# Optimization experiments

Hardware: AMD Instinct MI355X
Metric: run time of the kernel (lower is better)

## Reference

```python
import jax, jax.numpy as jnp
import numpy as np

T, B, D_IN, H = 512, 256, 64, 128


def _normc(key, shape):
    w = jax.random.normal(key, shape, dtype=jnp.float32)
    return w / jnp.sqrt(jnp.sum(w * w, axis=1, keepdims=True))


def setup_inputs() -> dict:
    key = jax.random.key(0)
    ks = jax.random.split(key, 8)
    state = jax.random.normal(ks[0], (T, B, D_IN), dtype=jnp.float32)
    # PyTorch LSTMCell params: weight_ih [4H, in], weight_hh [4H, H], biases [4H]
    s = 1.0 / np.sqrt(H)
    W_ih0 = jax.random.uniform(ks[1], (4 * H, D_IN), minval=-s, maxval=s, dtype=jnp.float32)
    W_hh0 = jax.random.uniform(ks[2], (4 * H, H), minval=-s, maxval=s, dtype=jnp.float32)
    b_ih0 = jnp.zeros((4 * H,), jnp.float32)
    b_hh0 = jnp.zeros((4 * H,), jnp.float32)
    W_ih1 = jax.random.uniform(ks[3], (4 * H, H), minval=-s, maxval=s, dtype=jnp.float32)
    W_hh1 = jax.random.uniform(ks[4], (4 * H, H), minval=-s, maxval=s, dtype=jnp.float32)
    b_ih1 = jnp.zeros((4 * H,), jnp.float32)
    b_hh1 = jnp.zeros((4 * H,), jnp.float32)
    # normc-initialized output head (rows normalized to unit norm, zero bias)
    W_out = _normc(ks[5], (1, H))
    b_out = jnp.zeros((1,), jnp.float32)
    return dict(state=state, W_ih0=W_ih0, W_hh0=W_hh0, b_ih0=b_ih0, b_hh0=b_hh0,
                W_ih1=W_ih1, W_hh1=W_hh1, b_ih1=b_ih1, b_hh1=b_hh1,
                W_out=W_out, b_out=b_out)


def _lstm_cell(x, h, c, W_ih, W_hh, b_ih, b_hh):
    # gates: [B, 4H], chunk order i, f, g, o (PyTorch convention)
    g = x @ W_ih.T + b_ih + h @ W_hh.T + b_hh
    i, f, gg, o = jnp.split(g, 4, axis=-1)
    i = jax.nn.sigmoid(i)
    f = jax.nn.sigmoid(f)
    gg = jnp.tanh(gg)
    o = jax.nn.sigmoid(o)
    c2 = f * c + i * gg
    h2 = o * jnp.tanh(c2)
    return h2, c2


def reference(state, W_ih0, W_hh0, b_ih0, b_hh0, W_ih1, W_hh1, b_ih1, b_hh1, W_out, b_out):
    Bsz = state.shape[1]
    Hd = W_hh0.shape[1]
    z = jnp.zeros((Bsz, Hd), state.dtype)

    def step(carry, x_t):
        h0, c0, h1, c1 = carry
        h0, c0 = _lstm_cell(x_t, h0, c0, W_ih0, W_hh0, b_ih0, b_hh0)
        h1, c1 = _lstm_cell(h0, h1, c1, W_ih1, W_hh1, b_ih1, b_hh1)
        v_t = h1 @ W_out.T + b_out  # [B, 1]
        return (h0, c0, h1, c1), v_t

    _, values = jax.lax.scan(step, (z, z, z, z), state)
    return values  # [T, B, 1]
```

## Files before the change

kernel.cpp:

```cpp
#include <hip/hip_runtime.h>


#define T_STEPS 512
#define BATCH   256
#define DIN     64
#define GROUP   16
#define NGRP    (T_STEPS / GROUP)

typedef _Float16 half8 __attribute__((ext_vector_type(8)));
typedef float    f32x4 __attribute__((ext_vector_type(4)));

#define LOG2E  1.44269504088896f
#define LOG2E2 2.88539008177793f

#define WH_IH0 0
#define WH_HH0 32768
#define WH_IH1 98304
#define WH_HH1 163840
#define WH_X2     229376
#define WH_SLAB2  8617984
#define WB_FLAG2  50790400
#define WS2_TOTAL 50823168
#define WH_SLAB1  229376
#define WB_FLAG1  34013184
#define WS1_TOTAL 34045952
#define WS0XH_TOTAL ((size_t)(WH_X2 + 8388608) * 2)

__global__ void prep_weights(const float* __restrict__ wih0,
                             const float* __restrict__ whh0,
                             const float* __restrict__ wih1,
                             const float* __restrict__ whh1,
                             _Float16* __restrict__ ws) {
    int idx = blockIdx.x * 256 + threadIdx.x;
    float v; int row;
    if (idx < 32768)       { row = idx >> 6;             v = wih0[idx]; }
    else if (idx < 98304)  { row = (idx - 32768) >> 7;   v = whh0[idx - 32768]; }
    else if (idx < 163840) { row = (idx - 98304) >> 7;   v = wih1[idx - 98304]; }
    else                   { row = (idx - 163840) >> 7;  v = whh1[idx - 163840]; }
    float sc = ((row >> 7) == 2) ? LOG2E2 : LOG2E;
    ws[idx] = (_Float16)(v * sc);
}

__global__ void prep_state(const float* __restrict__ s, _Float16* __restrict__ d) {
    int i = (blockIdx.x * 256 + threadIdx.x) * 8;
    f32x4 a = *(const f32x4*)(s + i);
    f32x4 b = *(const f32x4*)(s + i + 4);
    half8 h;
    h[0]=(_Float16)a[0]; h[1]=(_Float16)a[1]; h[2]=(_Float16)a[2]; h[3]=(_Float16)a[3];
    h[4]=(_Float16)b[0]; h[5]=(_Float16)b[1]; h[6]=(_Float16)b[2]; h[7]=(_Float16)b[3];
    *(half8*)(d + i) = h;
}

__device__ __forceinline__ float sig2(float y) {
    return __builtin_amdgcn_rcpf(1.0f + __builtin_amdgcn_exp2f(-y));
}
__device__ __forceinline__ float tanh2(float y2) {
    return 1.0f - 2.0f * __builtin_amdgcn_rcpf(1.0f + __builtin_amdgcn_exp2f(y2));
}
__device__ __forceinline__ float tanh_c(float c) {
    return 1.0f - 2.0f * __builtin_amdgcn_rcpf(1.0f + __builtin_amdgcn_exp2f(c * LOG2E2));
}

#define PIPE_LDS_BYTES ((65536 + 4096 + 128) * 2)

template<bool XH>
__global__ __launch_bounds__(512, 1) void lstm_pipe(
        const float* __restrict__ state32, const _Float16* __restrict__ wsw,
        const float* __restrict__ b_ih0, const float* __restrict__ b_hh0,
        const float* __restrict__ b_ih1, const float* __restrict__ b_hh1,
        const float* __restrict__ w_out, const float* __restrict__ b_out,
        _Float16* __restrict__ slab, int* __restrict__ flags,
        const _Float16* __restrict__ xh, float* __restrict__ out) {
    extern __shared__ _Float16 lds[];
    _Float16* wrec  = lds;
    _Float16* hdb   = lds + 65536;
    _Float16* woutl = lds + 69632;

    const int tid  = threadIdx.x;
    const int w    = tid >> 6;
    const int lane = tid & 63;
    const int col  = lane & 15;
    const int quad = lane >> 4;
    const bool producer = blockIdx.x < 16;
    const int tile = blockIdx.x & 15;
    const int rowbase = tile * 16;
    const int j0 = w * 16 + col;

    const _Float16* wrg = wsw + (producer ? WH_HH0 : WH_HH1);
    #pragma unroll
    for (int it = 0; it < 16; ++it) {
        int flat = (it * 512 + tid) * 8;
        int r = flat >> 7, chunk = (flat >> 3) & 15;
        *(half8*)(wrec + r * 128 + ((chunk ^ (r & 15)) * 8)) = *(const half8*)(wrg + flat);
    }
    {
        half8 z;
        #pragma unroll
        for (int jj = 0; jj < 8; ++jj) z[jj] = (_Float16)0.0f;
        *(half8*)(hdb + tid * 8) = z;
    }
    if (!producer && tid < 128) woutl[tid] = (_Float16)w_out[tid];

    half8 wresf[4][4];
    float bias[4];
    #pragma unroll
    for (int nt = 0; nt < 4; ++nt) {
        int j = nt * 128 + j0;
        float sc = (nt == 2) ? LOG2E2 : LOG2E;
        if (producer) {
            #pragma unroll
            for (int kt = 0; kt < 2; ++kt)
                wresf[nt][kt] = *(const half8*)(wsw + WH_IH0 + j * 64 + kt * 32 + quad * 8);
            bias[nt] = (b_ih0[j] + b_hh0[j]) * sc;
        } else {
            #pragma unroll
            for (int kt = 0; kt < 4; ++kt)
                wresf[nt][kt] = *(const half8*)(wsw + WH_IH1 + j * 128 + kt * 32 + quad * 8);
            bias[nt] = (b_ih1[j] + b_hh1[j]) * sc;
        }
    }
    const float bout = b_out[0];

    int swz[4], hoff[4], w0off[4];
    #pragma unroll
    for (int kt = 0; kt < 4; ++kt) {
        swz[kt]  = ((kt * 4 + quad) ^ col) * 8;
        hoff[kt] = col * 128 + swz[kt];
    }
    #pragma unroll
    for (int i = 0; i < 4; ++i) {
        int row = quad * 4 + i;
        w0off[i] = row * 128 + (((2 * w + (col >> 3)) ^ row) * 8) + (col & 7);
    }
    float cc[4] = {0.f, 0.f, 0.f, 0.f};

    __syncthreads();

    if (producer) {
        const _Float16* xph = xh + (size_t)(rowbase + col) * DIN + quad * 8;
        const float*    xpf = state32 + (size_t)(rowbase + col) * DIN + quad * 8;
        half8 nxh0, nxh1;
        f32x4 nxf0, nxf1, nxf2, nxf3;
        if constexpr (XH) {
            nxh0 = *(const half8*)(xph);
            nxh1 = *(const half8*)(xph + 32);
        } else {
            nxf0 = *(const f32x4*)(xpf);      nxf1 = *(const f32x4*)(xpf + 4);
            nxf2 = *(const f32x4*)(xpf + 32); nxf3 = *(const f32x4*)(xpf + 36);
        }
        _Float16 hh[4];

        #pragma unroll 1
        for (int t = 0; t < T_STEPS; ++t) {
            const int pbo = (t & 1) * 2048, cbo = pbo ^ 2048;
            const int lt = t & (GROUP - 1);
            __syncthreads();

            if (lt == 0) {
                if (t > 0 && tid == 0)
                    __hip_atomic_store(flags + (t / GROUP - 1) * 16 + tile, t / GROUP,
                                       __ATOMIC_RELEASE, __HIP_MEMORY_SCOPE_AGENT);
            } else {
                _Float16* slabP = slab + (size_t)((t - 1) * 16 + tile) * 2048;
                #pragma unroll
                for (int i = 0; i < 4; ++i)
                    slabP[(quad * 4 + i) * 128 + j0] = hh[i];
            }

            half8 ax0, ax1;
            if constexpr (XH) { ax0 = nxh0; ax1 = nxh1; }
            else {
                #pragma unroll
                for (int jj = 0; jj < 4; ++jj) {
                    ax0[jj]   = (_Float16)nxf0[jj]; ax0[jj+4] = (_Float16)nxf1[jj];
                    ax1[jj]   = (_Float16)nxf2[jj]; ax1[jj+4] = (_Float16)nxf3[jj];
                }
            }
            half8 ah[4];
            #pragma unroll
            for (int kt = 0; kt < 4; ++kt)
                ah[kt] = *(const half8*)(hdb + pbo + hoff[kt]);

            f32x4 acc[4];
            #pragma unroll
            for (int nt = 0; nt < 4; ++nt) {
                f32x4 b = {bias[nt], bias[nt], bias[nt], bias[nt]};
                acc[nt] = b;
            }
            #pragma unroll
            for (int kt = 0; kt < 4; ++kt)
                #pragma unroll
                for (int nt = 0; nt < 4; ++nt) {
                    half8 bfr = *(const half8*)(wrec + nt * 16384 + j0 * 128 + swz[kt]);
                    acc[nt] = __builtin_amdgcn_mfma_f32_16x16x32_f16(ah[kt], bfr, acc[nt], 0, 0, 0);
                }
            #pragma unroll
            for (int kt = 0; kt < 2; ++kt) {
                half8 axk = kt ? ax1 : ax0;
                #pragma unroll
                for (int nt = 0; nt < 4; ++nt)
                    acc[nt] = __builtin_amdgcn_mfma_f32_16x16x32_f16(axk, wresf[nt][kt], acc[nt], 0, 0, 0);
            }

            {
                int tn = (t + 1 < T_STEPS) ? t + 1 : t;
                if constexpr (XH) {
                    const _Float16* xq = xph + (size_t)tn * (BATCH * DIN);
                    nxh0 = *(const half8*)(xq);
                    nxh1 = *(const half8*)(xq + 32);
                } else {
                    const float* xq = xpf + (size_t)tn * (BATCH * DIN);
                    nxf0 = *(const f32x4*)(xq);      nxf1 = *(const f32x4*)(xq + 4);
                    nxf2 = *(const f32x4*)(xq + 32); nxf3 = *(const f32x4*)(xq + 36);
                }
            }

            _Float16* slabT = slab + (size_t)(t * 16 + tile) * 2048;
            #pragma unroll
            for (int i = 0; i < 4; ++i) {
                float ig = sig2(acc[0][i]);
                float fg = sig2(acc[1][i]);
                float gg = tanh2(acc[2][i]);
                float og = sig2(acc[3][i]);
                float c  = fg * cc[i] + ig * gg;
                cc[i] = c;
                _Float16 hf = (_Float16)(og * tanh_c(c));
                hdb[cbo + w0off[i]] = hf;
                if (lt == GROUP - 1)
                    slabT[(quad * 4 + i) * 128 + j0] = hf;
                else
                    hh[i] = hf;
            }
        }
        __syncthreads();
        if (tid == 0)
            __hip_atomic_store(flags + (NGRP - 1) * 16 + tile, NGRP,
                               __ATOMIC_RELEASE, __HIP_MEMORY_SCOPE_AGENT);
    } else {
        if (tid == 0) {
            while (__hip_atomic_load(flags + tile, __ATOMIC_ACQUIRE,
                                     __HIP_MEMORY_SCOPE_AGENT) < 1)
                __builtin_amdgcn_s_sleep(1);
        }
        __syncthreads();

        half8 curA[4], nextA[4];
        {
            const _Float16* s0 = slab + (size_t)tile * 2048;
            #pragma unroll
            for (int kt = 0; kt < 4; ++kt)
                curA[kt] = *(const half8*)(s0 + col * 128 + kt * 32 + quad * 8);
        }

        #pragma unroll 1
        for (int t = 0; t < T_STEPS; ++t) {
            const int pbo = (t & 1) * 2048, cbo = pbo ^ 2048;
            const int lt = t & (GROUP - 1);
            __syncthreads();

            half8 a1[4];
            #pragma unroll
            for (int kt = 0; kt < 4; ++kt)
                a1[kt] = *(const half8*)(hdb + pbo + hoff[kt]);

            f32x4 acc[4];
            #pragma unroll
            for (int nt = 0; nt < 4; ++nt) {
                f32x4 b = {bias[nt], bias[nt], bias[nt], bias[nt]};
                acc[nt] = b;
            }
            #pragma unroll
            for (int kt = 0; kt < 4; ++kt)
                #pragma unroll
                for (int nt = 0; nt < 4; ++nt) {
                    half8 bfr = *(const half8*)(wrec + nt * 16384 + j0 * 128 + swz[kt]);
                    acc[nt] = __builtin_amdgcn_mfma_f32_16x16x32_f16(a1[kt], bfr, acc[nt], 0, 0, 0);
                }
            #pragma unroll
            for (int kt = 0; kt < 4; ++kt)
                #pragma unroll
                for (int nt = 0; nt < 4; ++nt)
                    acc[nt] = __builtin_amdgcn_mfma_f32_16x16x32_f16(curA[kt], wresf[nt][kt], acc[nt], 0, 0, 0);

            if (lt == 12 && tid == 0) {
                int g1 = (t >> 4) + 1;
                if (g1 < NGRP) {
                    while (__hip_atomic_load(flags + g1 * 16 + tile, __ATOMIC_ACQUIRE,
                                             __HIP_MEMORY_SCOPE_AGENT) < g1 + 1)
                        __builtin_amdgcn_s_sleep(1);
                }
            }

            {
                int tn = (t + 1 < T_STEPS) ? t + 1 : t;
                const _Float16* sq = slab + (size_t)(tn * 16 + tile) * 2048;
                #pragma unroll
                for (int kt = 0; kt < 4; ++kt)
                    nextA[kt] = *(const half8*)(sq + col * 128 + kt * 32 + quad * 8);
            }

            #pragma unroll
            for (int i = 0; i < 4; ++i) {
                float ig = sig2(acc[0][i]);
                float fg = sig2(acc[1][i]);
                float gg = tanh2(acc[2][i]);
                float og = sig2(acc[3][i]);
                float c  = fg * cc[i] + ig * gg;
                cc[i] = c;
                hdb[cbo + w0off[i]] = (_Float16)(og * tanh_c(c));
            }

            if (w == 7) {
                f32x4 vh = {0.f, 0.f, 0.f, 0.f};
                #pragma unroll
                for (int kt = 0; kt < 4; ++kt) {
                    half8 av = *(const half8*)(hdb + pbo + hoff[kt]);
                    half8 bw = *(const half8*)(woutl + kt * 32 + quad * 8);
                    if (col != 0) {
                        #pragma unroll
                        for (int jj = 0; jj < 8; ++jj) bw[jj] = (_Float16)0.0f;
                    }
                    vh = __builtin_amdgcn_mfma_f32_16x16x32_f16(av, bw, vh, 0, 0, 0);
                }
                if (t > 0 && col == 0) {
                    f32x4 vo = {vh[0] + bout, vh[1] + bout, vh[2] + bout, vh[3] + bout};
                    *(f32x4*)(out + (size_t)(t - 1) * BATCH + rowbase + quad * 4) = vo;
                }
            }

            #pragma unroll
            for (int kt = 0; kt < 4; ++kt) curA[kt] = nextA[kt];
        }
        __syncthreads();
        if (w == 7) {
            const int fbo = (((T_STEPS - 1) & 1) ^ 1) * 2048;
            f32x4 vh = {0.f, 0.f, 0.f, 0.f};
            #pragma unroll
            for (int kt = 0; kt < 4; ++kt) {
                half8 av = *(const half8*)(hdb + fbo + hoff[kt]);
                half8 bw = *(const half8*)(woutl + kt * 32 + quad * 8);
                if (col != 0) {
                    #pragma unroll
                    for (int jj = 0; jj < 8; ++jj) bw[jj] = (_Float16)0.0f;
                }
                vh = __builtin_amdgcn_mfma_f32_16x16x32_f16(av, bw, vh, 0, 0, 0);
            }
            if (col == 0) {
                f32x4 vo = {vh[0] + bout, vh[1] + bout, vh[2] + bout, vh[3] + bout};
                *(f32x4*)(out + (size_t)(T_STEPS - 1) * BATCH + rowbase + quad * 4) = vo;
            }
        }
    }
}

#define MONO_LDS_BYTES ((73728 + 128) * 2)

template<bool XH>
__global__ __launch_bounds__(512, 2) void lstm_mono(
        const float* __restrict__ state32, const _Float16* __restrict__ wsw,
        const float* __restrict__ b_ih0, const float* __restrict__ b_hh0,
        const float* __restrict__ b_ih1, const float* __restrict__ b_hh1,
        const float* __restrict__ w_out, const float* __restrict__ b_out,
        float* __restrict__ out) {
    extern __shared__ _Float16 lds[];
    _Float16* whh1  = lds;
    _Float16* h0b   = lds + 65536;
    _Float16* h1b   = lds + 69632;
    _Float16* woutl = lds + 73728;

    const int tid  = threadIdx.x;
    const int w    = tid >> 6;
    const int lane = tid & 63;
    const int col  = lane & 15;
    const int quad = lane >> 4;
    const int rowbase = blockIdx.x * 16;
    const int j0 = w * 16 + col;

    const _Float16* whh1g = wsw + WH_HH1;
    #pragma unroll
    for (int it = 0; it < 16; ++it) {
        int flat = (it * 512 + tid) * 8;
        int r = flat >> 7, chunk = (flat >> 3) & 15;
        *(half8*)(whh1 + r * 128 + ((chunk ^ (r & 15)) * 8)) = *(const half8*)(whh1g + flat);
    }
    {
        half8 z;
        #pragma unroll
        for (int jj = 0; jj < 8; ++jj) z[jj] = (_Float16)0.0f;
        for (int i = tid * 8; i < 8192; i += 4096) *(half8*)(h0b + i) = z;
    }
    if (tid < 128) woutl[tid] = (_Float16)w_out[tid];

    half8 whh0f[4][4], wih1f[4][4];
    float bias0[4], bias1[4];
    #pragma unroll
    for (int nt = 0; nt < 4; ++nt) {
        int j = nt * 128 + j0;
        float sc = (nt == 2) ? LOG2E2 : LOG2E;
        #pragma unroll
        for (int kt = 0; kt < 4; ++kt) {
            whh0f[nt][kt] = *(const half8*)(wsw + WH_HH0 + j * 128 + kt * 32 + quad * 8);
            wih1f[nt][kt] = *(const half8*)(wsw + WH_IH1 + j * 128 + kt * 32 + quad * 8);
        }
        bias0[nt] = (b_ih0[j] + b_hh0[j]) * sc;
        bias1[nt] = (b_ih1[j] + b_hh1[j]) * sc;
    }
    const float bout = b_out[0];

    int swz[4], hoff[4], w0off[4];
    #pragma unroll
    for (int kt = 0; kt < 4; ++kt) {
        swz[kt]  = ((kt * 4 + quad) ^ col) * 8;
        hoff[kt] = col * 128 + swz[kt];
    }
    #pragma unroll
    for (int i = 0; i < 4; ++i) {
        int row = quad * 4 + i;
        w0off[i] = row * 128 + (((2 * w + (col >> 3)) ^ row) * 8) + (col & 7);
    }
    float c0[4] = {0.f,0.f,0.f,0.f}, c1[4] = {0.f,0.f,0.f,0.f};

    const _Float16* xph = wsw + WH_X2 + (size_t)(rowbase + col) * DIN + quad * 8;
    const float*    xpf = state32 + (size_t)(rowbase + col) * DIN + quad * 8;
    half8 nxh0, nxh1;
    f32x4 nxf0, nxf1, nxf2, nxf3;
    if constexpr (XH) {
        nxh0 = *(const half8*)(xph); nxh1 = *(const half8*)(xph + 32);
    } else {
        nxf0 = *(const f32x4*)(xpf);      nxf1 = *(const f32x4*)(xpf + 4);
        nxf2 = *(const f32x4*)(xpf + 32); nxf3 = *(const f32x4*)(xpf + 36);
// ... 73 lines not shown
        #pragma unroll
        for (int kt = 0; kt < 4; ++kt) {
            half8 a0 = *(const half8*)(h0b + cbo + hoff[kt]);
            half8 a1 = *(const half8*)(h1b + pbo + hoff[kt]);
            #pragma unroll
            for (int nt = 0; nt < 4; ++nt)
                acc[nt] = __builtin_amdgcn_mfma_f32_16x16x32_f16(a0, wih1f[nt][kt], acc[nt], 0, 0, 0);
            #pragma unroll
            for (int nt = 0; nt < 4; ++nt) {
                half8 bfr = *(const half8*)(whh1 + nt * 16384 + j0 * 128 + swz[kt]);
                acc[nt] = __builtin_amdgcn_mfma_f32_16x16x32_f16(a1, bfr, acc[nt], 0, 0, 0);
            }
        }
        #pragma unroll
        for (int i = 0; i < 4; ++i) {
            float ig = sig2(acc[0][i]);
            float fg = sig2(acc[1][i]);
            float gg = tanh2(acc[2][i]);
            float og = sig2(acc[3][i]);
            float c  = fg * c1[i] + ig * gg;
            c1[i] = c;
            h1b[cbo + w0off[i]] = (_Float16)(og * tanh_c(c));
        }
        if (w == 7) {
            f32x4 vh = {0.f, 0.f, 0.f, 0.f};
            #pragma unroll
            for (int kt = 0; kt < 4; ++kt) {
                half8 a1 = *(const half8*)(h1b + pbo + hoff[kt]);
                half8 bw = *(const half8*)(woutl + kt * 32 + quad * 8);
                if (col != 0) {
                    #pragma unroll
                    for (int jj = 0; jj < 8; ++jj) bw[jj] = (_Float16)0.0f;
                }
                vh = __builtin_amdgcn_mfma_f32_16x16x32_f16(a1, bw, vh, 0, 0, 0);
            }
            if (t > 0 && col == 0) {
                f32x4 vo = {vh[0] + bout, vh[1] + bout, vh[2] + bout, vh[3] + bout};
                *(f32x4*)(out + (size_t)(t - 1) * BATCH + rowbase + quad * 4) = vo;
            }
        }
    }
    __syncthreads();
    if (w == 7) {
        const int fbo = (((T_STEPS - 1) & 1) ^ 1) * 2048;
        f32x4 vh = {0.f, 0.f, 0.f, 0.f};
        #pragma unroll
        for (int kt = 0; kt < 4; ++kt) {
            half8 a1 = *(const half8*)(h1b + fbo + hoff[kt]);
            half8 bw = *(const half8*)(woutl + kt * 32 + quad * 8);
            if (col != 0) {
                #pragma unroll
                for (int jj = 0; jj < 8; ++jj) bw[jj] = (_Float16)0.0f;
            }
            vh = __builtin_amdgcn_mfma_f32_16x16x32_f16(a1, bw, vh, 0, 0, 0);
        }
        if (col == 0) {
            f32x4 vo = {vh[0] + bout, vh[1] + bout, vh[2] + bout, vh[3] + bout};
            *(f32x4*)(out + (size_t)(T_STEPS - 1) * BATCH + rowbase + quad * 4) = vo;
        }
    }
}

extern "C" void kernel_launch(void* const* d_in, const int* in_sizes, int n_in,
                              void* d_out, int out_size, void* d_ws, size_t ws_size,
                              hipStream_t stream) {
    const float* state = (const float*)d_in[0];
    const float* wih0  = (const float*)d_in[1];
    const float* whh0  = (const float*)d_in[2];
    const float* bih0  = (const float*)d_in[3];
    const float* bhh0  = (const float*)d_in[4];
    const float* wih1  = (const float*)d_in[5];
    const float* whh1  = (const float*)d_in[6];
    const float* bih1  = (const float*)d_in[7];
    const float* bhh1  = (const float*)d_in[8];
    const float* wout  = (const float*)d_in[9];
    const float* bout  = (const float*)d_in[10];
    _Float16* wsh = (_Float16*)d_ws;
    float* outp = (float*)d_out;

    prep_weights<<<896, 256, 0, stream>>>(wih0, whh0, wih1, whh1, wsh);

    if (ws_size >= WS2_TOTAL) {
        prep_state<<<4096, 256, 0, stream>>>(state, wsh + WH_X2);
        lstm_pipe<true><<<32, 512, PIPE_LDS_BYTES, stream>>>(
            state, wsh, bih0, bhh0, bih1, bhh1, wout, bout,
            wsh + WH_SLAB2, (int*)((char*)d_ws + WB_FLAG2), wsh + WH_X2, outp);
    } else if (ws_size >= WS1_TOTAL) {
        lstm_pipe<false><<<32, 512, PIPE_LDS_BYTES, stream>>>(
            state, wsh, bih0, bhh0, bih1, bhh1, wout, bout,
            wsh + WH_SLAB1, (int*)((char*)d_ws + WB_FLAG1), nullptr, outp);
    } else if (ws_size >= WS0XH_TOTAL) {
        prep_state<<<4096, 256, 0, stream>>>(state, wsh + WH_X2);
        lstm_mono<true><<<16, 512, MONO_LDS_BYTES, stream>>>(
            state, wsh, bih0, bhh0, bih1, bhh1, wout, bout, outp);
    } else {
        lstm_mono<false><<<16, 512, MONO_LDS_BYTES, stream>>>(
            state, wsh, bih0, bhh0, bih1, bhh1, wout, bout, outp);
    }
}
```

Measured before the change: 713.9 us.

## Split batch into 32 tiles of 8 rows across 64 pipelined workgroups

Doubles the number of producer/consumer workgroup pairs from 16 to 32, with each tile handling 8 batch rows instead of 16. The per-step recurrent chain per workgroup gets shorter and more CUs are used. The cost is that half of each 16-row MFMA tile is wasted on duplicated rows, and there are twice as many flags and slab writes. It also reorders the per-step work: slab prefetch is issued earlier, input MFMAs run before the recurrent ones, and the value-head MFMA rotates across waves with its weights kept in registers.

New measurement: 1.048 ms. +46.9%, slower.

```diff
diff --git a/kernel.cpp b/kernel.cpp
--- a/kernel.cpp
+++ b/kernel.cpp
@@ -6,6 +6,7 @@
 #define DIN     64
 #define GROUP   16
 #define NGRP    (T_STEPS / GROUP)
+#define NTILE   32
 
 typedef _Float16 half8 __attribute__((ext_vector_type(8)));
 typedef float    f32x4 __attribute__((ext_vector_type(4)));
@@ -61,7 +62,7 @@
     return 1.0f - 2.0f * __builtin_amdgcn_rcpf(1.0f + __builtin_amdgcn_exp2f(c * LOG2E2));
 }
 
-#define PIPE_LDS_BYTES ((65536 + 4096 + 128) * 2)
+#define PIPE_LDS_BYTES ((65536 + 2048 + 128) * 2)
 
 template<bool XH>
 __global__ __launch_bounds__(512, 1) void lstm_pipe(
@@ -74,16 +75,17 @@
     extern __shared__ _Float16 lds[];
     _Float16* wrec  = lds;
     _Float16* hdb   = lds + 65536;
-    _Float16* woutl = lds + 69632;
+    _Float16* woutl = lds + 67584;
 
     const int tid  = threadIdx.x;
     const int w    = tid >> 6;
     const int lane = tid & 63;
     const int col  = lane & 15;
+    const int colc = col & 7;
     const int quad = lane >> 4;
-    const bool producer = blockIdx.x < 16;
-    const int tile = blockIdx.x & 15;
-    const int rowbase = tile * 16;
+    const bool producer = blockIdx.x < NTILE;
+    const int tile = blockIdx.x & (NTILE - 1);
+    const int rowbase = tile * 8;
     const int j0 = w * 16 + col;
 
     const _Float16* wrg = wsw + (producer ? WH_HH0 : WH_HH1);
@@ -93,7 +95,7 @@
         int r = flat >> 7, chunk = (flat >> 3) & 15;
         *(half8*)(wrec + r * 128 + ((chunk ^ (r & 15)) * 8)) = *(const half8*)(wrg + flat);
     }
-    {
+    if (tid < 256) {
         half8 z;
         #pragma unroll
         for (int jj = 0; jj < 8; ++jj) z[jj] = (_Float16)0.0f;
@@ -121,24 +123,24 @@
     }
     const float bout = b_out[0];
 
-    int swz[4], hoff[4], w0off[4];
+    int swzW[4], hoffA[4], w0off[4];
     #pragma unroll
     for (int kt = 0; kt < 4; ++kt) {
-        swz[kt]  = ((kt * 4 + quad) ^ col) * 8;
-        hoff[kt] = col * 128 + swz[kt];
+        swzW[kt]  = ((kt * 4 + quad) ^ col) * 8;
+        hoffA[kt] = colc * 128 + (((kt * 4 + quad) ^ colc) * 8);
     }
     #pragma unroll
     for (int i = 0; i < 4; ++i) {
         int row = quad * 4 + i;
-        w0off[i] = row * 128 + (((2 * w + (col >> 3)) ^ row) * 8) + (col & 7);
+        w0off[i] = row * 128 + ((((2 * w + (col >> 3)) ^ row) & 15) * 8) + (col & 7);
     }
     float cc[4] = {0.f, 0.f, 0.f, 0.f};
 
     __syncthreads();
 
     if (producer) {
-        const _Float16* xph = xh + (size_t)(rowbase + col) * DIN + quad * 8;
-        const float*    xpf = state32 + (size_t)(rowbase + col) * DIN + quad * 8;
+        const _Float16* xph = xh + (size_t)(rowbase + colc) * DIN + quad * 8;
+        const float*    xpf = state32 + (size_t)(rowbase + colc) * DIN + quad * 8;
         half8 nxh0, nxh1;
         f32x4 nxf0, nxf1, nxf2, nxf3;
         if constexpr (XH) {
@@ -152,20 +154,9 @@
 
         #pragma unroll 1
         for (int t = 0; t < T_STEPS; ++t) {
-            const int pbo = (t & 1) * 2048, cbo = pbo ^ 2048;
+            const int pbo = (t & 1) << 10, cbo = pbo ^ 1024;
             const int lt = t & (GROUP - 1);
             __syncthreads();
-
-            if (lt == 0) {
-                if (t > 0 && tid == 0)
-                    __hip_atomic_store(flags + (t / GROUP - 1) * 16 + tile, t / GROUP,
-                                       __ATOMIC_RELEASE, __HIP_MEMORY_SCOPE_AGENT);
-            } else {
-                _Float16* slabP = slab + (size_t)((t - 1) * 16 + tile) * 2048;
-                #pragma unroll
-                for (int i = 0; i < 4; ++i)
-                    slabP[(quad * 4 + i) * 128 + j0] = hh[i];
-            }
 
             half8 ax0, ax1;
             if constexpr (XH) { ax0 = nxh0; ax1 = nxh1; }
@@ -175,31 +166,6 @@
                     ax0[jj]   = (_Float16)nxf0[jj]; ax0[jj+4] = (_Float16)nxf1[jj];
                     ax1[jj]   = (_Float16)nxf2[jj]; ax1[jj+4] = (_Float16)nxf3[jj];
                 }
-            }
-            half8 ah[4];
-            #pragma unroll
-            for (int kt = 0; kt < 4; ++kt)
-                ah[kt] = *(const half8*)(hdb + pbo + hoff[kt]);
-
-            f32x4 acc[4];
-            #pragma unroll
-            for (int nt = 0; nt < 4; ++nt) {
-                f32x4 b = {bias[nt], bias[nt], bias[nt], bias[nt]};
-                acc[nt] = b;
-            }
-            #pragma unroll
-            for (int kt = 0; kt < 4; ++kt)
-                #pragma unroll
-                for (int nt = 0; nt < 4; ++nt) {
-                    half8 bfr = *(const half8*)(wrec + nt * 16384 + j0 * 128 + swz[kt]);
-                    acc[nt] = __builtin_amdgcn_mfma_f32_16x16x32_f16(ah[kt], bfr, acc[nt], 0, 0, 0);
-                }
-            #pragma unroll
-            for (int kt = 0; kt < 2; ++kt) {
-                half8 axk = kt ? ax1 : ax0;
-                #pragma unroll
-                for (int nt = 0; nt < 4; ++nt)
-                    acc[nt] = __builtin_amdgcn_mfma_f32_16x16x32_f16(axk, wresf[nt][kt], acc[nt], 0, 0, 0);
             }
 
             {
@@ -214,29 +180,77 @@
                     nxf2 = *(const f32x4*)(xq + 32); nxf3 = *(const f32x4*)(xq + 36);
                 }
             }
-
-            _Float16* slabT = slab + (size_t)(t * 16 + tile) * 2048;
-            #pragma unroll
-            for (int i = 0; i < 4; ++i) {
-                float ig = sig2(acc[0][i]);
-                float fg = sig2(acc[1][i]);
-                float gg = tanh2(acc[2][i]);
-                float og = sig2(acc[3][i]);
-                float c  = fg * cc[i] + ig * gg;
-                cc[i] = c;
-                _Float16 hf = (_Float16)(og * tanh_c(c));
-                hdb[cbo + w0off[i]] = hf;
-                if (lt == GROUP - 1)
-                    slabT[(quad * 4 + i) * 128 + j0] = hf;
-                else
-                    hh[i] = hf;
+            if (lt == 0) {
+                if (t > 0 && tid == 0)
+                    __hip_atomic_store(flags + (t / GROUP - 1) * NTILE + tile, t / GROUP,
+                                       __ATOMIC_RELEASE, __HIP_MEMORY_SCOPE_AGENT);
+            } else if (quad < 2) {
+                _Float16* slabP = slab + (size_t)((t - 1) * NTILE + tile) * 1024;
+                #pragma unroll
+                for (int i = 0; i < 4; ++i)
+                    slabP[(quad * 4 + i) * 128 + j0] = hh[i];
+            }
+
+            half8 ah[4];
+            #pragma unroll
+            for (int kt = 0; kt < 4; ++kt)
+                ah[kt] = *(const half8*)(hdb + pbo + hoffA[kt]);
+
+            f32x4 acc[4];
+            #pragma unroll
+            for (int nt = 0; nt < 4; ++nt) {
+                f32x4 b = {bias[nt], bias[nt], bias[nt], bias[nt]};
+                acc[nt] = b;
+            }
+            #pragma unroll
+            for (int kt = 0; kt < 2; ++kt) {
+                half8 axk = kt ? ax1 : ax0;
+                #pragma unroll
+                for (int nt = 0; nt < 4; ++nt)
+                    acc[nt] = __builtin_amdgcn_mfma_f32_16x16x32_f16(axk, wresf[nt][kt], acc[nt], 0, 0, 0);
+            }
+            #pragma unroll
+            for (int kt = 0; kt < 4; ++kt)
+                #pragma unroll
+                for (int nt = 0; nt < 4; ++nt) {
+                    half8 bfr = *(const half8*)(wrec + nt * 16384 + j0 * 128 + swzW[kt]);
+                    acc[nt] = __builtin_amdgcn_mfma_f32_16x16x32_f16(ah[kt], bfr, acc[nt], 0, 0, 0);
+                }
+
+            if (quad < 2) {
+                _Float16* slabT = slab + (size_t)(t * NTILE + tile) * 1024;
+                #pragma unroll
+                for (int i = 0; i < 4; ++i) {
+                    float ig = sig2(acc[0][i]);
+                    float fg = sig2(acc[1][i]);
+                    float gg = tanh2(acc[2][i]);
+                    float og = sig2(acc[3][i]);
+                    float c  = fg * cc[i] + ig * gg;
+                    cc[i] = c;
+                    _Float16 hf = (_Float16)(og * tanh_c(c));
+                    hdb[cbo + w0off[i]] = hf;
+                    if (lt == GROUP - 1)
+                        slabT[(quad * 4 + i) * 128 + j0] = hf;
+                    else
+                        hh[i] = hf;
+                }
             }
         }
         __syncthreads();
         if (tid == 0)
-            __hip_atomic_store(flags + (NGRP - 1) * 16 + tile, NGRP,
+            __hip_atomic_store(flags + (NGRP - 1) * NTILE + tile, NGRP,
                                __ATOMIC_RELEASE, __HIP_MEMORY_SCOPE_AGENT);
     } else {
+        half8 bwf[4];
+        #pragma unroll
+        for (int kt = 0; kt < 4; ++kt) {
+            half8 bw = *(const half8*)(woutl + kt * 32 + quad * 8);
+            if (col != 0) {
+                #pragma unroll
+                for (int jj = 0; jj < 8; ++jj) bw[jj] = (_Float16)0.0f;
+            }
+            bwf[kt] = bw;
+        }
         if (tid == 0) {
             while (__hip_atomic_load(flags + tile, __ATOMIC_ACQUIRE,
                                      __HIP_MEMORY_SCOPE_AGENT) < 1)
@@ -246,22 +260,30 @@
 
         half8 curA[4], nextA[4];
         {
-            const _Float16* s0 = slab + (size_t)tile * 2048;
+            const _Float16* s0 = slab + (size_t)tile * 1024;
             #pragma unroll
             for (int kt = 0; kt < 4; ++kt)
-                curA[kt] = *(const half8*)(s0 + col * 128 + kt * 32 + quad * 8);
+                curA[kt] = *(const half8*)(s0 + colc * 128 + kt * 32 + quad * 8);
         }
 
         #pragma unroll 1
         for (int t = 0; t < T_STEPS; ++t) {
-            const int pbo = (t & 1) * 2048, cbo = pbo ^ 2048;
+            const int pbo = (t & 1) << 10, cbo = pbo ^ 1024;
             const int lt = t & (GROUP - 1);
             __syncthreads();
 
+            {
+                int tn = (t + 1 < T_STEPS) ? t + 1 : t;
+                const _Float16* sq = slab + (size_t)(tn * NTILE + tile) * 1024;
+                #pragma unroll
+                for (int kt = 0; kt < 4; ++kt)
+                    nextA[kt] = *(const half8*)(sq + colc * 128 + kt * 32 + quad * 8);
+            }
+
             half8 a1[4];
             #pragma unroll
             for (int kt = 0; kt < 4; ++kt)
-                a1[kt] = *(const half8*)(hdb + pbo + hoff[kt]);
+                a1[kt] = *(const half8*)(hdb + pbo + hoffA[kt]);
 
             f32x4 acc[4];
             #pragma unroll
@@ -272,59 +294,47 @@
             #pragma unroll
             for (int kt = 0; kt < 4; ++kt)
                 #pragma unroll
-                for (int nt = 0; nt < 4; ++nt) {
-                    half8 bfr = *(const half8*)(wrec + nt * 16384 + j0 * 128 + swz[kt]);
-                    acc[nt] = __builtin_amdgcn_mfma_f32_16x16x32_f16(a1[kt], bfr, acc[nt], 0, 0, 0);
-                }
-            #pragma unroll
-            for (int kt = 0; kt < 4; ++kt)
-                #pragma unroll
                 for (int nt = 0; nt < 4; ++nt)
                     acc[nt] = __builtin_amdgcn_mfma_f32_16x16x32_f16(curA[kt], wresf[nt][kt], acc[nt], 0, 0, 0);
+
+            if (w == (t & 7) && t > 0) {
+                f32x4 vh = {0.f, 0.f, 0.f, 0.f};
+                #pragma unroll
+                for (int kt = 0; kt < 4; ++kt)
+                    vh = __builtin_amdgcn_mfma_f32_16x16x32_f16(a1[kt], bwf[kt], vh, 0, 0, 0);
+                if (col == 0 && quad < 2) {
+                    f32x4 vo = {vh[0] + bout, vh[1] + bout, vh[2] + bout, vh[3] + bout};
+                    *(f32x4*)(out + (size_t)(t - 1) * BATCH + rowbase + quad * 4) = vo;
+                }
+            }
+
+            #pragma unroll
+            for (int kt = 0; kt < 4; ++kt)
+                #pragma unroll
+                for (int nt = 0; nt < 4; ++nt) {
+                    half8 bfr = *(const half8*)(wrec + nt * 16384 + j0 * 128 + swzW[kt]);
+                    acc[nt] = __builtin_amdgcn_mfma_f32_16x16x32_f16(a1[kt], bfr, acc[nt], 0, 0, 0);
+                }
 
             if (lt == 12 && tid == 0) {
                 int g1 = (t >> 4) + 1;
                 if (g1 < NGRP) {
-                    while (__hip_atomic_load(flags + g1 * 16 + tile, __ATOMIC_ACQUIRE,
+                    while (__hip_atomic_load(flags + g1 * NTILE + tile, __ATOMIC_ACQUIRE,
                                              __HIP_MEMORY_SCOPE_AGENT) < g1 + 1)
                         __builtin_amdgcn_s_sleep(1);
                 }
             }
 
-            {
-                int tn = (t + 1 < T_STEPS) ? t + 1 : t;
-                const _Float16* sq = slab + (size_t)(tn * 16 + tile) * 2048;
-                #pragma unroll
-                for (int kt = 0; kt < 4; ++kt)
-                    nextA[kt] = *(const half8*)(sq + col * 128 + kt * 32 + quad * 8);
-            }
-
-            #pragma unroll
-            for (int i = 0; i < 4; ++i) {
-                float ig = sig2(acc[0][i]);
-                float fg = sig2(acc[1][i]);
-                float gg = tanh2(acc[2][i]);
-                float og = sig2(acc[3][i]);
-                float c  = fg * cc[i] + ig * gg;
-                cc[i] = c;
-                hdb[cbo + w0off[i]] = (_Float16)(og * tanh_c(c));
-            }
-
-            if (w == 7) {
-                f32x4 vh = {0.f, 0.f, 0.f, 0.f};
-                #pragma unroll
-                for (int kt = 0; kt < 4; ++kt) {
-                    half8 av = *(const half8*)(hdb + pbo + hoff[kt]);
-                    half8 bw = *(const half8*)(woutl + kt * 32 + quad * 8);
-                    if (col != 0) {
-                        #pragma unroll
-                        for (int jj = 0; jj < 8; ++jj) bw[jj] = (_Float16)0.0f;
-                    }
-                    vh = __builtin_amdgcn_mfma_f32_16x16x32_f16(av, bw, vh, 0, 0, 0);
-                }
-                if (t > 0 && col == 0) {
-                    f32x4 vo = {vh[0] + bout, vh[1] + bout, vh[2] + bout, vh[3] + bout};
-                    *(f32x4*)(out + (size_t)(t - 1) * BATCH + rowbase + quad * 4) = vo;
+            if (quad < 2) {
+                #pragma unroll
+                for (int i = 0; i < 4; ++i) {
+                    float ig = sig2(acc[0][i]);
+                    float fg = sig2(acc[1][i]);
+                    float gg = tanh2(acc[2][i]);
+                    float og = sig2(acc[3][i]);
+                    float c  = fg * cc[i] + ig * gg;
+                    cc[i] = c;
+                    hdb[cbo + w0off[i]] = (_Float16)(og * tanh_c(c));
                 }
             }
 
@@ -333,19 +343,14 @@
         }
         __syncthreads();
         if (w == 7) {
-            const int fbo = (((T_STEPS - 1) & 1) ^ 1) * 2048;
+            const int fbo = (((T_STEPS - 1) & 1) ^ 1) << 10;
             f32x4 vh = {0.f, 0.f, 0.f, 0.f};
             #pragma unroll
             for (int kt = 0; kt < 4; ++kt) {
-                half8 av = *(const half8*)(hdb + fbo + hoff[kt]);
-                half8 bw = *(const half8*)(woutl + kt * 32 + quad * 8);
-                if (col != 0) {
-                    #pragma unroll
-                    for (int jj = 0; jj < 8; ++jj) bw[jj] = (_Float16)0.0f;
-                }
-                vh = __builtin_amdgcn_mfma_f32_16x16x32_f16(av, bw, vh, 0, 0, 0);
-            }
-            if (col == 0) {
+                half8 av = *(const half8*)(hdb + fbo + hoffA[kt]);
+                vh = __builtin_amdgcn_mfma_f32_16x16x32_f16(av, bwf[kt], vh, 0, 0, 0);
+            }
+            if (col == 0 && quad < 2) {
                 f32x4 vo = {vh[0] + bout, vh[1] + bout, vh[2] + bout, vh[3] + bout};
                 *(f32x4*)(out + (size_t)(T_STEPS - 1) * BATCH + rowbase + quad * 4) = vo;
             }
@@ -585,11 +590,11 @@
 
     if (ws_size >= WS2_TOTAL) {
         prep_state<<<4096, 256, 0, stream>>>(state, wsh + WH_X2);
-        lstm_pipe<true><<<32, 512, PIPE_LDS_BYTES, stream>>>(
+        lstm_pipe<true><<<2 * NTILE, 512, PIPE_LDS_BYTES, stream>>>(
             state, wsh, bih0, bhh0, bih1, bhh1, wout, bout,
             wsh + WH_SLAB2, (int*)((char*)d_ws + WB_FLAG2), wsh + WH_X2, outp);
     } else if (ws_size >= WS1_TOTAL) {
-        lstm_pipe<false><<<32, 512, PIPE_LDS_BYTES, stream>>>(
+        lstm_pipe<false><<<2 * NTILE, 512, PIPE_LDS_BYTES, stream>>>(
             state, wsh, bih0, bhh0, bih1, bhh1, wout, bout,
             wsh + WH_SLAB1, (int*)((char*)d_ws + WB_FLAG1), nullptr, outp);
     } else if (ws_size >= WS0XH_TOTAL) {
```

## Hold recurrent LSTM weights in AGPRs instead of LDS in pipelined kernel

Applied to the files above, without the earlier changes.

Each wave's slice of the recurrent weight matrices W_hh0/W_hh1 now lives in register fragments, pinned to accumulator registers with empty asm constraints, instead of being staged into a 128 KB swizzled LDS buffer and re-read every timestep. LDS shrinks to the small h double buffer. The output-head weights become per-lane register fragments, and the value-head MFMA reuses the already-loaded h fragments instead of re-reading LDS. Slab prefetch and the input-projection MFMAs are moved earlier so they overlap with latency. This removes per-step LDS traffic on the serial recurrence critical path, at the cost of much higher register pressure, which could cause spills.

Result: slower. 971.0 us (+36.0%).

```diff
diff --git a/kernel.cpp b/kernel.cpp
--- a/kernel.cpp
+++ b/kernel.cpp
@@ -61,7 +61,7 @@
     return 1.0f - 2.0f * __builtin_amdgcn_rcpf(1.0f + __builtin_amdgcn_exp2f(c * LOG2E2));
 }
 
-#define PIPE_LDS_BYTES ((65536 + 4096 + 128) * 2)
+#define PIPE_LDS_BYTES 8192
 
 template<bool XH>
 __global__ __launch_bounds__(512, 1) void lstm_pipe(
@@ -72,9 +72,7 @@
         _Float16* __restrict__ slab, int* __restrict__ flags,
         const _Float16* __restrict__ xh, float* __restrict__ out) {
     extern __shared__ _Float16 lds[];
-    _Float16* wrec  = lds;
-    _Float16* hdb   = lds + 65536;
-    _Float16* woutl = lds + 69632;
+    _Float16* hdb = lds;
 
     const int tid  = threadIdx.x;
     const int w    = tid >> 6;
@@ -86,22 +84,14 @@
     const int rowbase = tile * 16;
     const int j0 = w * 16 + col;
 
-    const _Float16* wrg = wsw + (producer ? WH_HH0 : WH_HH1);
-    #pragma unroll
-    for (int it = 0; it < 16; ++it) {
-        int flat = (it * 512 + tid) * 8;
-        int r = flat >> 7, chunk = (flat >> 3) & 15;
-        *(half8*)(wrec + r * 128 + ((chunk ^ (r & 15)) * 8)) = *(const half8*)(wrg + flat);
-    }
     {
         half8 z;
         #pragma unroll
         for (int jj = 0; jj < 8; ++jj) z[jj] = (_Float16)0.0f;
         *(half8*)(hdb + tid * 8) = z;
     }
-    if (!producer && tid < 128) woutl[tid] = (_Float16)w_out[tid];
-
-    half8 wresf[4][4];
+
+    half8 wrecf[4][4], wresf[4][4];
     float bias[4];
     #pragma unroll
     for (int nt = 0; nt < 4; ++nt) {
@@ -109,24 +99,43 @@
         float sc = (nt == 2) ? LOG2E2 : LOG2E;
         if (producer) {
             #pragma unroll
+            for (int kt = 0; kt < 4; ++kt)
+                wrecf[nt][kt] = *(const half8*)(wsw + WH_HH0 + j * 128 + kt * 32 + quad * 8);
+            #pragma unroll
             for (int kt = 0; kt < 2; ++kt)
                 wresf[nt][kt] = *(const half8*)(wsw + WH_IH0 + j * 64 + kt * 32 + quad * 8);
             bias[nt] = (b_ih0[j] + b_hh0[j]) * sc;
         } else {
             #pragma unroll
-            for (int kt = 0; kt < 4; ++kt)
+            for (int kt = 0; kt < 4; ++kt) {
+                wrecf[nt][kt] = *(const half8*)(wsw + WH_HH1 + j * 128 + kt * 32 + quad * 8);
                 wresf[nt][kt] = *(const half8*)(wsw + WH_IH1 + j * 128 + kt * 32 + quad * 8);
+            }
             bias[nt] = (b_ih1[j] + b_hh1[j]) * sc;
         }
     }
+    #pragma unroll
+    for (int nt = 0; nt < 4; ++nt) {
+        #pragma unroll
+        for (int kt = 0; kt < 4; ++kt)
+            asm volatile("" : "+a"(wrecf[nt][kt]));
+        #pragma unroll
+        for (int kt = 0; kt < 2; ++kt)
+            asm volatile("" : "+a"(wresf[nt][kt]));
+    }
+    if (!producer) {
+        #pragma unroll
+        for (int nt = 0; nt < 4; ++nt)
+            #pragma unroll
+            for (int kt = 2; kt < 4; ++kt)
+                asm volatile("" : "+a"(wresf[nt][kt]));
+    }
     const float bout = b_out[0];
 
-    int swz[4], hoff[4], w0off[4];
-    #pragma unroll
-    for (int kt = 0; kt < 4; ++kt) {
-        swz[kt]  = ((kt * 4 + quad) ^ col) * 8;
-        hoff[kt] = col * 128 + swz[kt];
-    }
+    int hoff[4], w0off[4];
+    #pragma unroll
+    for (int kt = 0; kt < 4; ++kt)
+        hoff[kt] = col * 128 + (((kt * 4 + quad) ^ col) * 8);
     #pragma unroll
     for (int i = 0; i < 4; ++i) {
         int row = quad * 4 + i;
@@ -152,20 +161,9 @@
 
         #pragma unroll 1
         for (int t = 0; t < T_STEPS; ++t) {
-            const int pbo = (t & 1) * 2048, cbo = pbo ^ 2048;
+            const int pbo = (t & 1) << 11, cbo = pbo ^ 2048;
             const int lt = t & (GROUP - 1);
             __syncthreads();
-
-            if (lt == 0) {
-                if (t > 0 && tid == 0)
-                    __hip_atomic_store(flags + (t / GROUP - 1) * 16 + tile, t / GROUP,
-                                       __ATOMIC_RELEASE, __HIP_MEMORY_SCOPE_AGENT);
-            } else {
-                _Float16* slabP = slab + (size_t)((t - 1) * 16 + tile) * 2048;
-                #pragma unroll
-                for (int i = 0; i < 4; ++i)
-                    slabP[(quad * 4 + i) * 128 + j0] = hh[i];
-            }
 
             half8 ax0, ax1;
             if constexpr (XH) { ax0 = nxh0; ax1 = nxh1; }
@@ -176,32 +174,6 @@
                     ax1[jj]   = (_Float16)nxf2[jj]; ax1[jj+4] = (_Float16)nxf3[jj];
                 }
             }
-            half8 ah[4];
-            #pragma unroll
-            for (int kt = 0; kt < 4; ++kt)
-                ah[kt] = *(const half8*)(hdb + pbo + hoff[kt]);
-
-            f32x4 acc[4];
-            #pragma unroll
-            for (int nt = 0; nt < 4; ++nt) {
-                f32x4 b = {bias[nt], bias[nt], bias[nt], bias[nt]};
-                acc[nt] = b;
-            }
-            #pragma unroll
-            for (int kt = 0; kt < 4; ++kt)
-                #pragma unroll
-                for (int nt = 0; nt < 4; ++nt) {
-                    half8 bfr = *(const half8*)(wrec + nt * 16384 + j0 * 128 + swz[kt]);
-                    acc[nt] = __builtin_amdgcn_mfma_f32_16x16x32_f16(ah[kt], bfr, acc[nt], 0, 0, 0);
-                }
-            #pragma unroll
-            for (int kt = 0; kt < 2; ++kt) {
-                half8 axk = kt ? ax1 : ax0;
-                #pragma unroll
-                for (int nt = 0; nt < 4; ++nt)
-                    acc[nt] = __builtin_amdgcn_mfma_f32_16x16x32_f16(axk, wresf[nt][kt], acc[nt], 0, 0, 0);
-            }
-
             {
                 int tn = (t + 1 < T_STEPS) ? t + 1 : t;
                 if constexpr (XH) {
@@ -214,6 +186,40 @@
                     nxf2 = *(const f32x4*)(xq + 32); nxf3 = *(const f32x4*)(xq + 36);
                 }
             }
+            if (lt == 0) {
+                if (t > 0 && tid == 0)
+                    __hip_atomic_store(flags + (t / GROUP - 1) * 16 + tile, t / GROUP,
+                                       __ATOMIC_RELEASE, __HIP_MEMORY_SCOPE_AGENT);
+            } else {
+                _Float16* slabP = slab + (size_t)((t - 1) * 16 + tile) * 2048;
+                #pragma unroll
+                for (int i = 0; i < 4; ++i)
+                    slabP[(quad * 4 + i) * 128 + j0] = hh[i];
+            }
+
+            half8 ah[4];
+            #pragma unroll
+            for (int kt = 0; kt < 4; ++kt)
+                ah[kt] = *(const half8*)(hdb + pbo + hoff[kt]);
+
+            f32x4 acc[4];
+            #pragma unroll
+            for (int nt = 0; nt < 4; ++nt) {
+                f32x4 b = {bias[nt], bias[nt], bias[nt], bias[nt]};
+                acc[nt] = b;
+            }
+            #pragma unroll
+            for (int kt = 0; kt < 2; ++kt) {
+                half8 axk = kt ? ax1 : ax0;
+                #pragma unroll
+                for (int nt = 0; nt < 4; ++nt)
+                    acc[nt] = __builtin_amdgcn_mfma_f32_16x16x32_f16(axk, wresf[nt][kt], acc[nt], 0, 0, 0);
+            }
+            #pragma unroll
+            for (int kt = 0; kt < 4; ++kt)
+                #pragma unroll
+                for (int nt = 0; nt < 4; ++nt)
+                    acc[nt] = __builtin_amdgcn_mfma_f32_16x16x32_f16(ah[kt], wrecf[nt][kt], acc[nt], 0, 0, 0);
 
             _Float16* slabT = slab + (size_t)(t * 16 + tile) * 2048;
             #pragma unroll
@@ -237,6 +243,24 @@
             __hip_atomic_store(flags + (NGRP - 1) * 16 + tile, NGRP,
                                __ATOMIC_RELEASE, __HIP_MEMORY_SCOPE_AGENT);
     } else {
+        half8 bwf[4];
+        #pragma unroll
+        for (int kt = 0; kt < 4; ++kt) {
+            half8 bw;
+            if (col == 0) {
+                f32x4 wa = *(const f32x4*)(w_out + kt * 32 + quad * 8);
+                f32x4 wb = *(const f32x4*)(w_out + kt * 32 + quad * 8 + 4);
+                #pragma unroll
+                for (int jj = 0; jj < 4; ++jj) {
+                    bw[jj]     = (_Float16)wa[jj];
+                    bw[jj + 4] = (_Float16)wb[jj];
+                }
+            } else {
+                #pragma unroll
+                for (int jj = 0; jj < 8; ++jj) bw[jj] = (_Float16)0.0f;
+            }
+            bwf[kt] = bw;
+        }
         if (tid == 0) {
             while (__hip_atomic_load(flags + tile, __ATOMIC_ACQUIRE,
                                      __HIP_MEMORY_SCOPE_AGENT) < 1)
@@ -254,9 +278,17 @@
 
         #pragma unroll 1
         for (int t = 0; t < T_STEPS; ++t) {
-            const int pbo = (t & 1) * 2048, cbo = pbo ^ 2048;
+            const int pbo = (t & 1) << 11, cbo = pbo ^ 2048;
             const int lt = t & (GROUP - 1);
             __syncthreads();
+
+            {
+                int tn = (t + 1 < T_STEPS) ? t + 1 : t;
+                const _Float16* sq = slab + (size_t)(tn * 16 + tile) * 2048;
+                #pragma unroll
+                for (int kt = 0; kt < 4; ++kt)
+                    nextA[kt] = *(const half8*)(sq + col * 128 + kt * 32 + quad * 8);
+            }
 
             half8 a1[4];
             #pragma unroll
@@ -272,15 +304,25 @@
             #pragma unroll
             for (int kt = 0; kt < 4; ++kt)
                 #pragma unroll
-                for (int nt = 0; nt < 4; ++nt) {
-                    half8 bfr = *(const half8*)(wrec + nt * 16384 + j0 * 128 + swz[kt]);
-                    acc[nt] = __builtin_amdgcn_mfma_f32_16x16x32_f16(a1[kt], bfr, acc[nt], 0, 0, 0);
-                }
-            #pragma unroll
-            for (int kt = 0; kt < 4; ++kt)
-                #pragma unroll
                 for (int nt = 0; nt < 4; ++nt)
                     acc[nt] = __builtin_amdgcn_mfma_f32_16x16x32_f16(curA[kt], wresf[nt][kt], acc[nt], 0, 0, 0);
+
+            if (w == 7 && t > 0) {
+                f32x4 vh = {0.f, 0.f, 0.f, 0.f};
+                #pragma unroll
+                for (int kt = 0; kt < 4; ++kt)
+                    vh = __builtin_amdgcn_mfma_f32_16x16x32_f16(a1[kt], bwf[kt], vh, 0, 0, 0);
+                if (col == 0) {
+                    f32x4 vo = {vh[0] + bout, vh[1] + bout, vh[2] + bout, vh[3] + bout};
+                    *(f32x4*)(out + (size_t)(t - 1) * BATCH + rowbase + quad * 4) = vo;
+                }
+            }
+
+            #pragma unroll
+            for (int kt = 0; kt < 4; ++kt)
+                #pragma unroll
+                for (int nt = 0; nt < 4; ++nt)
+                    acc[nt] = __builtin_amdgcn_mfma_f32_16x16x32_f16(a1[kt], wrecf[nt][kt], acc[nt], 0, 0, 0);
 
             if (lt == 12 && tid == 0) {
                 int g1 = (t >> 4) + 1;
@@ -289,14 +331,6 @@
                                              __HIP_MEMORY_SCOPE_AGENT) < g1 + 1)
                         __builtin_amdgcn_s_sleep(1);
                 }
-            }
-
-            {
-                int tn = (t + 1 < T_STEPS) ? t + 1 : t;
-                const _Float16* sq = slab + (size_t)(tn * 16 + tile) * 2048;
-                #pragma unroll
-                for (int kt = 0; kt < 4; ++kt)
-                    nextA[kt] = *(const half8*)(sq + col * 128 + kt * 32 + quad * 8);
             }
 
             #pragma unroll
@@ -310,40 +344,17 @@
                 hdb[cbo + w0off[i]] = (_Float16)(og * tanh_c(c));
             }
 
-            if (w == 7) {
-                f32x4 vh = {0.f, 0.f, 0.f, 0.f};
-                #pragma unroll
-                for (int kt = 0; kt < 4; ++kt) {
-                    half8 av = *(const half8*)(hdb + pbo + hoff[kt]);
-                    half8 bw = *(const half8*)(woutl + kt * 32 + quad * 8);
-                    if (col != 0) {
-                        #pragma unroll
-                        for (int jj = 0; jj < 8; ++jj) bw[jj] = (_Float16)0.0f;
-                    }
-                    vh = __builtin_amdgcn_mfma_f32_16x16x32_f16(av, bw, vh, 0, 0, 0);
-                }
-                if (t > 0 && col == 0) {
-                    f32x4 vo = {vh[0] + bout, vh[1] + bout, vh[2] + bout, vh[3] + bout};
-                    *(f32x4*)(out + (size_t)(t - 1) * BATCH + rowbase + quad * 4) = vo;
-                }
-            }
-
             #pragma unroll
             for (int kt = 0; kt < 4; ++kt) curA[kt] = nextA[kt];
         }
         __syncthreads();
         if (w == 7) {
-            const int fbo = (((T_STEPS - 1) & 1) ^ 1) * 2048;
+            const int fbo = (((T_STEPS - 1) & 1) ^ 1) << 11;
             f32x4 vh = {0.f, 0.f, 0.f, 0.f};
             #pragma unroll
             for (int kt = 0; kt < 4; ++kt) {
                 half8 av = *(const half8*)(hdb + fbo + hoff[kt]);
-                half8 bw = *(const half8*)(woutl + kt * 32 + quad * 8);
-                if (col != 0) {
-                    #pragma unroll
-                    for (int jj = 0; jj < 8; ++jj) bw[jj] = (_Float16)0.0f;
-                }
-                vh = __builtin_amdgcn_mfma_f32_16x16x32_f16(av, bw, vh, 0, 0, 0);
+                vh = __builtin_amdgcn_mfma_f32_16x16x32_f16(av, bwf[kt], vh, 0, 0, 0);
             }
             if (col == 0) {
                 f32x4 vo = {vh[0] + bout, vh[1] + bout, vh[2] + bout, vh[3] + bout};
```

## Split gate accumulators and reorder LSTM step to shorten recurrent critical path

Applied to the files above, without the earlier changes.

Each time step now accumulates the input projection and the recurrent projection into separate accumulators, putting the MFMAs that do not depend on the hidden state first, and sums the two at the end. In the producer, the slab stores and flag release move after the next-x prefetch. In the consumer, the next slab prefetch moves to the top of the step, and the output head reuses the already-loaded hidden fragments instead of reloading them from LDS. The aim is to overlap latency and shorten the serial dependency chain, at the cost of extra accumulator registers and a vector add.

Result: slower. 983.5 us (+37.8%).

```diff
diff --git a/kernel.cpp b/kernel.cpp
--- a/kernel.cpp
+++ b/kernel.cpp
@@ -152,20 +152,9 @@
 
         #pragma unroll 1
         for (int t = 0; t < T_STEPS; ++t) {
-            const int pbo = (t & 1) * 2048, cbo = pbo ^ 2048;
+            const int pbo = (t & 1) << 11, cbo = pbo ^ 2048;
             const int lt = t & (GROUP - 1);
             __syncthreads();
-
-            if (lt == 0) {
-                if (t > 0 && tid == 0)
-                    __hip_atomic_store(flags + (t / GROUP - 1) * 16 + tile, t / GROUP,
-                                       __ATOMIC_RELEASE, __HIP_MEMORY_SCOPE_AGENT);
-            } else {
-                _Float16* slabP = slab + (size_t)((t - 1) * 16 + tile) * 2048;
-                #pragma unroll
-                for (int i = 0; i < 4; ++i)
-                    slabP[(quad * 4 + i) * 128 + j0] = hh[i];
-            }
 
             half8 ax0, ax1;
             if constexpr (XH) { ax0 = nxh0; ax1 = nxh1; }
@@ -175,31 +164,6 @@
                     ax0[jj]   = (_Float16)nxf0[jj]; ax0[jj+4] = (_Float16)nxf1[jj];
                     ax1[jj]   = (_Float16)nxf2[jj]; ax1[jj+4] = (_Float16)nxf3[jj];
                 }
-            }
-            half8 ah[4];
-            #pragma unroll
-            for (int kt = 0; kt < 4; ++kt)
-                ah[kt] = *(const half8*)(hdb + pbo + hoff[kt]);
-
-            f32x4 acc[4];
-            #pragma unroll
-            for (int nt = 0; nt < 4; ++nt) {
-                f32x4 b = {bias[nt], bias[nt], bias[nt], bias[nt]};
-                acc[nt] = b;
-            }
-            #pragma unroll
-            for (int kt = 0; kt < 4; ++kt)
-                #pragma unroll
-                for (int nt = 0; nt < 4; ++nt) {
-                    half8 bfr = *(const half8*)(wrec + nt * 16384 + j0 * 128 + swz[kt]);
-                    acc[nt] = __builtin_amdgcn_mfma_f32_16x16x32_f16(ah[kt], bfr, acc[nt], 0, 0, 0);
-                }
-            #pragma unroll
-            for (int kt = 0; kt < 2; ++kt) {
-                half8 axk = kt ? ax1 : ax0;
-                #pragma unroll
-                for (int nt = 0; nt < 4; ++nt)
-                    acc[nt] = __builtin_amdgcn_mfma_f32_16x16x32_f16(axk, wresf[nt][kt], acc[nt], 0, 0, 0);
             }
 
             {
@@ -214,6 +178,47 @@
                     nxf2 = *(const f32x4*)(xq + 32); nxf3 = *(const f32x4*)(xq + 36);
                 }
             }
+            if (lt == 0) {
+                if (t > 0 && tid == 0)
+                    __hip_atomic_store(flags + (t / GROUP - 1) * 16 + tile, t / GROUP,
+                                       __ATOMIC_RELEASE, __HIP_MEMORY_SCOPE_AGENT);
+            } else {
+                _Float16* slabP = slab + (size_t)((t - 1) * 16 + tile) * 2048;
+                #pragma unroll
+                for (int i = 0; i < 4; ++i)
+                    slabP[(quad * 4 + i) * 128 + j0] = hh[i];
+            }
+
+            half8 ah[4];
+            #pragma unroll
+            for (int kt = 0; kt < 4; ++kt)
+                ah[kt] = *(const half8*)(hdb + pbo + hoff[kt]);
+
+            f32x4 accI[4], accR[4];
+            #pragma unroll
+            for (int nt = 0; nt < 4; ++nt) {
+                f32x4 b = {bias[nt], bias[nt], bias[nt], bias[nt]};
+                accI[nt] = b;
+                f32x4 z = {0.f, 0.f, 0.f, 0.f};
+                accR[nt] = z;
+            }
+            #pragma unroll
+            for (int kt = 0; kt < 2; ++kt) {
+                half8 axk = kt ? ax1 : ax0;
+                #pragma unroll
+                for (int nt = 0; nt < 4; ++nt)
+                    accI[nt] = __builtin_amdgcn_mfma_f32_16x16x32_f16(axk, wresf[nt][kt], accI[nt], 0, 0, 0);
+            }
+            #pragma unroll
+            for (int kt = 0; kt < 4; ++kt)
+                #pragma unroll
+                for (int nt = 0; nt < 4; ++nt) {
+                    half8 bfr = *(const half8*)(wrec + nt * 16384 + j0 * 128 + swz[kt]);
+                    accR[nt] = __builtin_amdgcn_mfma_f32_16x16x32_f16(ah[kt], bfr, accR[nt], 0, 0, 0);
+                }
+            f32x4 acc[4];
+            #pragma unroll
+            for (int nt = 0; nt < 4; ++nt) acc[nt] = accI[nt] + accR[nt];
 
             _Float16* slabT = slab + (size_t)(t * 16 + tile) * 2048;
             #pragma unroll
@@ -254,33 +259,64 @@
 
         #pragma unroll 1
         for (int t = 0; t < T_STEPS; ++t) {
-            const int pbo = (t & 1) * 2048, cbo = pbo ^ 2048;
+            const int pbo = (t & 1) << 11, cbo = pbo ^ 2048;
             const int lt = t & (GROUP - 1);
             __syncthreads();
 
+            {
+                int tn = (t + 1 < T_STEPS) ? t + 1 : t;
+                const _Float16* sq = slab + (size_t)(tn * 16 + tile) * 2048;
+                #pragma unroll
+                for (int kt = 0; kt < 4; ++kt)
+                    nextA[kt] = *(const half8*)(sq + col * 128 + kt * 32 + quad * 8);
+            }
+
             half8 a1[4];
             #pragma unroll
             for (int kt = 0; kt < 4; ++kt)
                 a1[kt] = *(const half8*)(hdb + pbo + hoff[kt]);
 
-            f32x4 acc[4];
+            f32x4 accI[4], accR[4];
             #pragma unroll
             for (int nt = 0; nt < 4; ++nt) {
                 f32x4 b = {bias[nt], bias[nt], bias[nt], bias[nt]};
-                acc[nt] = b;
-            }
+                accI[nt] = b;
+                f32x4 z = {0.f, 0.f, 0.f, 0.f};
+                accR[nt] = z;
+            }
+            #pragma unroll
+            for (int kt = 0; kt < 4; ++kt)
+                #pragma unroll
+                for (int nt = 0; nt < 4; ++nt)
+                    accI[nt] = __builtin_amdgcn_mfma_f32_16x16x32_f16(curA[kt], wresf[nt][kt], accI[nt], 0, 0, 0);
+
+            if (w == 7 && t > 0) {
+                f32x4 vh = {0.f, 0.f, 0.f, 0.f};
+                #pragma unroll
+                for (int kt = 0; kt < 4; ++kt) {
+                    half8 bw = *(const half8*)(woutl + kt * 32 + quad * 8);
+                    if (col != 0) {
+                        #pragma unroll
+                        for (int jj = 0; jj < 8; ++jj) bw[jj] = (_Float16)0.0f;
+                    }
+                    vh = __builtin_amdgcn_mfma_f32_16x16x32_f16(a1[kt], bw, vh, 0, 0, 0);
+                }
+                if (col == 0) {
+                    f32x4 vo = {vh[0] + bout, vh[1] + bout, vh[2] + bout, vh[3] + bout};
+                    *(f32x4*)(out + (size_t)(t - 1) * BATCH + rowbase + quad * 4) = vo;
+                }
+            }
+
             #pragma unroll
             for (int kt = 0; kt < 4; ++kt)
                 #pragma unroll
                 for (int nt = 0; nt < 4; ++nt) {
                     half8 bfr = *(const half8*)(wrec + nt * 16384 + j0 * 128 + swz[kt]);
-                    acc[nt] = __builtin_amdgcn_mfma_f32_16x16x32_f16(a1[kt], bfr, acc[nt], 0, 0, 0);
-                }
-            #pragma unroll
-            for (int kt = 0; kt < 4; ++kt)
-                #pragma unroll
-                for (int nt = 0; nt < 4; ++nt)
-                    acc[nt] = __builtin_amdgcn_mfma_f32_16x16x32_f16(curA[kt], wresf[nt][kt], acc[nt], 0, 0, 0);
+                    accR[nt] = __builtin_amdgcn_mfma_f32_16x16x32_f16(a1[kt], bfr, accR[nt], 0, 0, 0);
+                }
+            f32x4 acc[4];
+            #pragma unroll
+            for (int nt = 0; nt < 4; ++nt) acc[nt] = accI[nt] + accR[nt];
 
             if (lt == 12 && tid == 0) {
                 int g1 = (t >> 4) + 1;
@@ -289,14 +325,6 @@
                                              __HIP_MEMORY_SCOPE_AGENT) < g1 + 1)
                         __builtin_amdgcn_s_sleep(1);
                 }
-            }
-
-            {
-                int tn = (t + 1 < T_STEPS) ? t + 1 : t;
-                const _Float16* sq = slab + (size_t)(tn * 16 + tile) * 2048;
-                #pragma unroll
-                for (int kt = 0; kt < 4; ++kt)
-                    nextA[kt] = *(const half8*)(sq + col * 128 + kt * 32 + quad * 8);
             }
 
             #pragma unroll
@@ -310,30 +338,12 @@
                 hdb[cbo + w0off[i]] = (_Float16)(og * tanh_c(c));
             }
 
-            if (w == 7) {
-                f32x4 vh = {0.f, 0.f, 0.f, 0.f};
-                #pragma unroll
-                for (int kt = 0; kt < 4; ++kt) {
-                    half8 av = *(const half8*)(hdb + pbo + hoff[kt]);
-                    half8 bw = *(const half8*)(woutl + kt * 32 + quad * 8);
-                    if (col != 0) {
-                        #pragma unroll
-                        for (int jj = 0; jj < 8; ++jj) bw[jj] = (_Float16)0.0f;
-                    }
-                    vh = __builtin_amdgcn_mfma_f32_16x16x32_f16(av, bw, vh, 0, 0, 0);
-                }
-                if (t > 0 && col == 0) {
-                    f32x4 vo = {vh[0] + bout, vh[1] + bout, vh[2] + bout, vh[3] + bout};
-                    *(f32x4*)(out + (size_t)(t - 1) * BATCH + rowbase + quad * 4) = vo;
-                }
-            }
-
             #pragma unroll
             for (int kt = 0; kt < 4; ++kt) curA[kt] = nextA[kt];
         }
         __syncthreads();
         if (w == 7) {
-            const int fbo = (((T_STEPS - 1) & 1) ^ 1) * 2048;
+            const int fbo = (((T_STEPS - 1) & 1) ^ 1) << 11;
             f32x4 vh = {0.f, 0.f, 0.f, 0.f};
             #pragma unroll
             for (int kt = 0; kt < 4; ++kt) {
```
